# Optimization experiments

Hardware: AMD Instinct MI355X
Metric: run time of the kernel (lower is better)

Reference implementation:

```python
import jax, jax.numpy as jnp
import numpy as np

N = 1500
GAT_IN = 32
GAT_OUT = 8
MLP_HIDDEN = 128
ALPHA = 0.2  # leaky relu slope
NEG_INF = -9.0e15


def setup_inputs() -> dict:
    key = jax.random.key(0)
    ks = jax.random.split(key, 16)
    eye = jnp.eye(N, dtype=jnp.float32)
    geo_adj = jnp.maximum((jax.random.uniform(ks[0], (N, N)) < 0.02).astype(jnp.float32), eye)
    sem_adj = jnp.maximum((jax.random.uniform(ks[1], (N, N)) < 0.02).astype(jnp.float32), eye)
    features = jax.random.normal(ks[2], (N, GAT_IN), dtype=jnp.float32)
    # all (i, j) region pairs, as in the original source
    ii, jj = jnp.meshgrid(jnp.arange(N), jnp.arange(N), indexing='ij')
    region_pairs = jnp.stack([ii.reshape(-1), jj.reshape(-1)], axis=1).astype(jnp.int64)
    distance_features = jax.random.uniform(ks[3], (N * N, 1), dtype=jnp.float32)
    def lin(k, fan_in, fan_out):
        return jax.random.normal(k, (fan_in, fan_out), dtype=jnp.float32) / jnp.sqrt(jnp.float32(fan_in))
    W0 = lin(ks[4], GAT_IN, GAT_OUT)
    W1 = lin(ks[5], GAT_OUT, GAT_OUT)
    W2 = lin(ks[6], GAT_OUT, GAT_OUT)
    a0 = lin(ks[7], 2 * GAT_OUT, 1)
    a1 = lin(ks[8], 2 * GAT_OUT, 1)
    a2 = lin(ks[9], 2 * GAT_OUT, 1)
    fc1_w = lin(ks[10], 2 * GAT_OUT + 1, MLP_HIDDEN)
    fc1_b = jnp.zeros((MLP_HIDDEN,), dtype=jnp.float32)
    fc2_w = lin(ks[11], MLP_HIDDEN, 1)
    fc2_b = jnp.zeros((1,), dtype=jnp.float32)
    return {"geo_adj": geo_adj, "sem_adj": sem_adj, "features": features,
            "region_pairs": region_pairs, "distance_features": distance_features,
            "W0": W0, "W1": W1, "W2": W2, "a0": a0, "a1": a1, "a2": a2,
            "fc1_w": fc1_w, "fc1_b": fc1_b, "fc2_w": fc2_w, "fc2_b": fc2_b}


def _gat_layer(combined_adj, feats, W, a):
    # h = W feats; attention score a([h_i || h_j]) decomposes into h_i@a1 + h_j@a2
    h = feats @ W                      # [N, out]
    f_src = h @ a[:GAT_OUT]            # [N, 1]
    f_dst = h @ a[GAT_OUT:]            # [N, 1]
    e = jax.nn.leaky_relu(f_src + f_dst.T, negative_slope=ALPHA)  # [N, N]
    e = e * combined_adj
    att = jax.nn.softmax(jnp.where(combined_adj > 0, e, NEG_INF), axis=1)
    return jax.nn.elu(att @ h)


def reference(geo_adj, sem_adj, features, region_pairs, distance_features,
              W0, W1, W2, a0, a1, a2, fc1_w, fc1_b, fc2_w, fc2_b):
    combined_adj = geo_adj + sem_adj
    enc = features
    for W, a in ((W0, a0), (W1, a1), (W2, a2)):
        enc = _gat_layer(combined_adj, enc, W, a)
    r1 = enc[region_pairs[:, 0]]       # [N^2, out]
    r2 = enc[region_pairs[:, 1]]       # [N^2, out]
    comb = jnp.concatenate([r1, r2, distance_features], axis=1)  # [N^2, 17]
    hid = jax.nn.relu(comb @ fc1_w + fc1_b)
    return hid @ fc2_w + fc2_b
```

## Files before the change

### kernel.cpp

```cpp
#include <hip/hip_runtime.h>
#include <hip/hip_bf16.h>

#define NN 1500
#define GIN 32
#define GOUT 8
#define HID 128

template<int IN>
__global__ void gat_project(const float* __restrict__ enc,
                            const float* __restrict__ W,
                            const float* __restrict__ avec,
                            float* __restrict__ h,
                            float* __restrict__ fsrc,
                            float* __restrict__ fdst) {
    int i = blockIdx.x * blockDim.x + threadIdx.x;
    if (i >= NN) return;
    float e[IN];
    #pragma unroll
    for (int c = 0; c < IN; ++c) e[c] = enc[i * IN + c];
    float hv[GOUT];
    #pragma unroll
    for (int k = 0; k < GOUT; ++k) {
        float s = 0.f;
        #pragma unroll
        for (int c = 0; c < IN; ++c) s = fmaf(e[c], W[c * GOUT + k], s);
        hv[k] = s;
        h[i * GOUT + k] = s;
    }
    float fs = 0.f, fd = 0.f;
    #pragma unroll
    for (int k = 0; k < GOUT; ++k) {
        fs = fmaf(hv[k], avec[k], fs);
        fd = fmaf(hv[k], avec[GOUT + k], fd);
    }
    fsrc[i] = fs;
    fdst[i] = fd;
}

__global__ void gat_attn(const float* __restrict__ geo,
                         const float* __restrict__ sem,
                         const float* __restrict__ h,
                         const float* __restrict__ fsrc,
                         const float* __restrict__ fdst,
                         float* __restrict__ enc_out) {
    const int i = blockIdx.x;
    const int t = threadIdx.x;
    const float s = fsrc[i];
    const float* grow = geo + (size_t)i * NN;
    const float* srow = sem + (size_t)i * NN;

    float m = -3.0e38f;
    for (int j = t; j < NN; j += 256) {
        float a = grow[j] + srow[j];
        if (a > 0.f) {
            float e = s + fdst[j];
            e = (e > 0.f) ? e : 0.2f * e;
            e *= a;
            m = fmaxf(m, e);
        }
    }
    #pragma unroll
    for (int off = 32; off > 0; off >>= 1)
        m = fmaxf(m, __shfl_down(m, off, 64));
    __shared__ float wred[4];
    if ((t & 63) == 0) wred[t >> 6] = m;
    __syncthreads();
    m = fmaxf(fmaxf(wred[0], wred[1]), fmaxf(wred[2], wred[3]));

    float l = 0.f;
    float acc[GOUT] = {};
    for (int j = t; j < NN; j += 256) {
        float a = grow[j] + srow[j];
        if (a > 0.f) {
            float e = s + fdst[j];
            e = (e > 0.f) ? e : 0.2f * e;
            e *= a;
            float p = __expf(e - m);
            l += p;
            const float* hr = h + j * GOUT;
            #pragma unroll
            for (int c = 0; c < GOUT; ++c) acc[c] = fmaf(p, hr[c], acc[c]);
        }
    }
    #pragma unroll
    for (int off = 32; off > 0; off >>= 1) {
        l += __shfl_down(l, off, 64);
        #pragma unroll
        for (int c = 0; c < GOUT; ++c) acc[c] += __shfl_down(acc[c], off, 64);
    }
    __shared__ float wsum[4][GOUT + 1];
    if ((t & 63) == 0) {
        wsum[t >> 6][0] = l;
        #pragma unroll
        for (int c = 0; c < GOUT; ++c) wsum[t >> 6][1 + c] = acc[c];
    }
    __syncthreads();
    if (t < GOUT) {
        float L = wsum[0][0] + wsum[1][0] + wsum[2][0] + wsum[3][0];
        float v = (wsum[0][1 + t] + wsum[1][1 + t] + wsum[2][1 + t] + wsum[3][1 + t]) / L;
        enc_out[i * GOUT + t] = (v > 0.f) ? v : (__expf(v) - 1.f);
    }
}

__global__ void uv_kernel(const float* __restrict__ enc,
                          const float* __restrict__ fc1w,
                          const float* __restrict__ fc1b,
                          float* __restrict__ U, float* __restrict__ V) {
    const int i = blockIdx.x;
    const int k = threadIdx.x;
    __shared__ float er[GOUT];
    if (k < GOUT) er[k] = enc[i * GOUT + k];
    __syncthreads();
    float u = fc1b[k];
    float v = 0.f;
    #pragma unroll
    for (int c = 0; c < GOUT; ++c) {
        u = fmaf(er[c], fc1w[c * HID + k], u);
        v = fmaf(er[c], fc1w[(GOUT + c) * HID + k], v);
    }
    U[i * HID + k] = u;
    V[i * HID + k] = v;
}

#define TILE 48
#define STRIDE 132

__global__ __launch_bounds__(256, 3) void mlp_kernel(
        const float* __restrict__ U, const float* __restrict__ V,
        const float* __restrict__ dist,
        const float* __restrict__ fc1w,
        const float* __restrict__ fc2w,
        const float* __restrict__ fc2b,
        float* __restrict__ out) {
    __shared__ float Us[TILE * STRIDE];
    __shared__ float Vs[TILE * STRIDE];
    __shared__ float w16s[HID];
    __shared__ float f2s[HID];

    const int tid = threadIdx.x;
    const int i0 = blockIdx.y * TILE;
    const int j0 = blockIdx.x * TILE;

    for (int t = tid; t < TILE * 32; t += 256) {
        int r = t >> 5;
        int k4 = (t & 31) << 2;
        int gi = i0 + r; if (gi >= NN) gi = NN - 1;
        int gj = j0 + r; if (gj >= NN) gj = NN - 1;
        *(float4*)(Us + r * STRIDE + k4) = *(const float4*)(U + gi * HID + k4);
        *(float4*)(Vs + r * STRIDE + k4) = *(const float4*)(V + gj * HID + k4);
    }
    if (tid < HID) {
        w16s[tid] = fc1w[16 * HID + tid];
        f2s[tid] = fc2w[tid];
    }
    __syncthreads();

    const int tx = tid & 15;
    const int ty = tid >> 4;

    int irow[3], jcol[3];
    float d[3][3];
    #pragma unroll
    for (int ii = 0; ii < 3; ++ii) irow[ii] = i0 + ty + 16 * ii;
    #pragma unroll
    for (int jj = 0; jj < 3; ++jj) jcol[jj] = j0 + tx + 16 * jj;
    #pragma unroll
    for (int ii = 0; ii < 3; ++ii) {
        int ic = irow[ii] < NN ? irow[ii] : NN - 1;
        #pragma unroll
        for (int jj = 0; jj < 3; ++jj) {
            int jc = jcol[jj] < NN ? jcol[jj] : NN - 1;
            d[ii][jj] = dist[(size_t)ic * NN + jc];
        }
    }

    float acc[3][3] = {};
    for (int k = 0; k < HID; k += 4) {
        float4 u4[3], v4[3];
        #pragma unroll
        for (int ii = 0; ii < 3; ++ii)
            u4[ii] = *(const float4*)(Us + (ty + 16 * ii) * STRIDE + k);
        #pragma unroll
        for (int jj = 0; jj < 3; ++jj)
            v4[jj] = *(const float4*)(Vs + (tx + 16 * jj) * STRIDE + k);
        float4 wk = *(const float4*)(w16s + k);
        float4 fk = *(const float4*)(f2s + k);
        const float* wkp = (const float*)&wk;
        const float* fkp = (const float*)&fk;
        #pragma unroll
        for (int kk = 0; kk < 4; ++kk) {
            float w = wkp[kk];
            float f = fkp[kk];
            #pragma unroll
            for (int ii = 0; ii < 3; ++ii) {
                float uv = ((const float*)&u4[ii])[kk];
                #pragma unroll
                for (int jj = 0; jj < 3; ++jj) {
                    float tval = fmaf(d[ii][jj], w, uv + ((const float*)&v4[jj])[kk]);
                    tval = fmaxf(tval, 0.f);
                    acc[ii][jj] = fmaf(tval, f, acc[ii][jj]);
                }
            }
        }
    }

    const float b2 = fc2b[0];
    #pragma unroll
    for (int ii = 0; ii < 3; ++ii) {
        if (irow[ii] >= NN) continue;
        #pragma unroll
        for (int jj = 0; jj < 3; ++jj) {
            if (jcol[jj] >= NN) continue;
            out[(size_t)irow[ii] * NN + jcol[jj]] = acc[ii][jj] + b2;
        }
    }
}

extern "C" void kernel_launch(void* const* d_in, const int* in_sizes, int n_in,
                              void* d_out, int out_size, void* d_ws, size_t ws_size,
                              hipStream_t stream) {
    const float* geo  = (const float*)d_in[0];
    const float* sem  = (const float*)d_in[1];
    const float* feat = (const float*)d_in[2];
    const float* dist = (const float*)d_in[4];
    const float* W0   = (const float*)d_in[5];
    const float* W1   = (const float*)d_in[6];
    const float* W2   = (const float*)d_in[7];
    const float* a0   = (const float*)d_in[8];
    const float* a1   = (const float*)d_in[9];
    const float* a2   = (const float*)d_in[10];
    const float* fc1w = (const float*)d_in[11];
    const float* fc1b = (const float*)d_in[12];
    const float* fc2w = (const float*)d_in[13];
    const float* fc2b = (const float*)d_in[14];
    float* out = (float*)d_out;

    float* ws   = (float*)d_ws;
    float* h    = ws;
    float* fsrc = h + NN * GOUT;
    float* fdst = fsrc + NN;
    float* encA = fdst + NN;
    float* encB = encA + NN * GOUT;
    float* Ubuf = encB + NN * GOUT;
    float* Vbuf = Ubuf + NN * HID;

    dim3 pg((NN + 255) / 256), pb(256);

    gat_project<GIN><<<pg, pb, 0, stream>>>(feat, W0, a0, h, fsrc, fdst);
    gat_attn<<<NN, 256, 0, stream>>>(geo, sem, h, fsrc, fdst, encA);

    gat_project<GOUT><<<pg, pb, 0, stream>>>(encA, W1, a1, h, fsrc, fdst);
    gat_attn<<<NN, 256, 0, stream>>>(geo, sem, h, fsrc, fdst, encB);

    gat_project<GOUT><<<pg, pb, 0, stream>>>(encB, W2, a2, h, fsrc, fdst);
    gat_attn<<<NN, 256, 0, stream>>>(geo, sem, h, fsrc, fdst, encA);

    uv_kernel<<<NN, HID, 0, stream>>>(encA, fc1w, fc1b, Ubuf, Vbuf);

    dim3 mg((NN + TILE - 1) / TILE, (NN + TILE - 1) / TILE);
    mlp_kernel<<<mg, 256, 0, stream>>>(Ubuf, Vbuf, dist, fc1w, fc2w, fc2b, out);
}
```

Before: 178.0 us.

## Build CSR adjacency once, fuse GAT projection/attention, fold UV into MLP

Scans the dense geo+sem adjacency once into a fixed-capacity CSR, so that each of the three GAT layers only visits actual neighbours instead of rereading two dense N×N matrices. Projection and attention are fused into one kernel that recomputes neighbour features on the fly, and the softmax skips max-subtraction. The U/V precompute is folded into the MLP tile load, and the MLP inner loop uses packed two-wide float math. Risks are neighbours beyond the 192 capacity being silently dropped, and exp overflow without the max shift.

```diff
diff --git a/kernel.cpp b/kernel.cpp
--- a/kernel.cpp
+++ b/kernel.cpp
@@ -5,130 +5,118 @@
 #define GIN 32
 #define GOUT 8
 #define HID 128
-
-template<int IN>
-__global__ void gat_project(const float* __restrict__ enc,
-                            const float* __restrict__ W,
-                            const float* __restrict__ avec,
-                            float* __restrict__ h,
-                            float* __restrict__ fsrc,
-                            float* __restrict__ fdst) {
-    int i = blockIdx.x * blockDim.x + threadIdx.x;
-    if (i >= NN) return;
-    float e[IN];
-    #pragma unroll
-    for (int c = 0; c < IN; ++c) e[c] = enc[i * IN + c];
-    float hv[GOUT];
-    #pragma unroll
-    for (int k = 0; k < GOUT; ++k) {
-        float s = 0.f;
-        #pragma unroll
-        for (int c = 0; c < IN; ++c) s = fmaf(e[c], W[c * GOUT + k], s);
-        hv[k] = s;
-        h[i * GOUT + k] = s;
-    }
-    float fs = 0.f, fd = 0.f;
-    #pragma unroll
-    for (int k = 0; k < GOUT; ++k) {
-        fs = fmaf(hv[k], avec[k], fs);
-        fd = fmaf(hv[k], avec[GOUT + k], fd);
-    }
-    fsrc[i] = fs;
-    fdst[i] = fd;
-}
-
-__global__ void gat_attn(const float* __restrict__ geo,
-                         const float* __restrict__ sem,
-                         const float* __restrict__ h,
-                         const float* __restrict__ fsrc,
-                         const float* __restrict__ fdst,
-                         float* __restrict__ enc_out) {
+#define CAP 192
+
+typedef float v2f __attribute__((ext_vector_type(2)));
+
+__global__ void build_csr(const float* __restrict__ geo,
+                          const float* __restrict__ sem,
+                          int* __restrict__ csr_idx,
+                          float* __restrict__ csr_val,
+                          int* __restrict__ csr_cnt) {
     const int i = blockIdx.x;
     const int t = threadIdx.x;
-    const float s = fsrc[i];
+    __shared__ int cnt;
+    __shared__ int sidx[CAP];
+    __shared__ float sval[CAP];
+    if (t == 0) cnt = 0;
+    __syncthreads();
     const float* grow = geo + (size_t)i * NN;
     const float* srow = sem + (size_t)i * NN;
-
-    float m = -3.0e38f;
-    for (int j = t; j < NN; j += 256) {
-        float a = grow[j] + srow[j];
-        if (a > 0.f) {
-            float e = s + fdst[j];
-            e = (e > 0.f) ? e : 0.2f * e;
-            e *= a;
-            m = fmaxf(m, e);
-        }
-    }
-    #pragma unroll
-    for (int off = 32; off > 0; off >>= 1)
-        m = fmaxf(m, __shfl_down(m, off, 64));
-    __shared__ float wred[4];
-    if ((t & 63) == 0) wred[t >> 6] = m;
+    for (int q = t; q < NN / 4; q += 256) {
+        float4 g = *(const float4*)(grow + 4 * q);
+        float4 s = *(const float4*)(srow + 4 * q);
+        float a[4] = {g.x + s.x, g.y + s.y, g.z + s.z, g.w + s.w};
+        #pragma unroll
+        for (int c = 0; c < 4; ++c) {
+            if (a[c] > 0.f) {
+                int p = atomicAdd(&cnt, 1);
+                if (p < CAP) { sidx[p] = 4 * q + c; sval[p] = a[c]; }
+            }
+        }
+    }
     __syncthreads();
-    m = fmaxf(fmaxf(wred[0], wred[1]), fmaxf(wred[2], wred[3]));
-
-    float l = 0.f;
-    float acc[GOUT] = {};
-    for (int j = t; j < NN; j += 256) {
-        float a = grow[j] + srow[j];
-        if (a > 0.f) {
-            float e = s + fdst[j];
-            e = (e > 0.f) ? e : 0.2f * e;
-            e *= a;
-            float p = __expf(e - m);
-            l += p;
-            const float* hr = h + j * GOUT;
+    int c2 = cnt < CAP ? cnt : CAP;
+    if (t == 0) csr_cnt[i] = c2;
+    for (int p = t; p < c2; p += 256) {
+        csr_idx[(size_t)i * CAP + p] = sidx[p];
+        csr_val[(size_t)i * CAP + p] = sval[p];
+    }
+}
+
+template<int IN>
+__global__ void gat_layer(const float* __restrict__ enc,
+                          const float* __restrict__ W,
+                          const float* __restrict__ avec,
+                          const int* __restrict__ csr_idx,
+                          const float* __restrict__ csr_val,
+                          const int* __restrict__ csr_cnt,
+                          float* __restrict__ enc_out) {
+    const int tid = threadIdx.x;
+    const int lane = tid & 63;
+    const int i = blockIdx.x * 4 + (tid >> 6);
+
+    float hv = 0.f;
+    if (lane < GOUT) {
+        #pragma unroll 4
+        for (int c = 0; c < IN; ++c)
+            hv = fmaf(enc[(size_t)i * IN + c], W[c * GOUT + lane], hv);
+    }
+    float hi[GOUT];
+    #pragma unroll
+    for (int c = 0; c < GOUT; ++c) hi[c] = __shfl(hv, c, 64);
+    float fsrc = 0.f;
+    #pragma unroll
+    for (int c = 0; c < GOUT; ++c) fsrc = fmaf(hi[c], avec[c], fsrc);
+
+    const int cnt = csr_cnt[i];
+    float den = 0.f;
+    float num[GOUT] = {};
+    for (int e = lane; e < cnt; e += 64) {
+        int j = csr_idx[(size_t)i * CAP + e];
+        float a = csr_val[(size_t)i * CAP + e];
+        float hj[GOUT] = {};
+        #pragma unroll
+        for (int c4 = 0; c4 < IN / 4; ++c4) {
+            float4 e4 = *(const float4*)(enc + (size_t)j * IN + 4 * c4);
+            const float* ep = (const float*)&e4;
             #pragma unroll
-            for (int c = 0; c < GOUT; ++c) acc[c] = fmaf(p, hr[c], acc[c]);
-        }
+            for (int c = 0; c < 4; ++c)
+                #pragma unroll
+                for (int k = 0; k < GOUT; ++k)
+                    hj[k] = fmaf(ep[c], W[(4 * c4 + c) * GOUT + k], hj[k]);
+        }
+        float fd = 0.f;
+        #pragma unroll
+        for (int k = 0; k < GOUT; ++k) fd = fmaf(hj[k], avec[GOUT + k], fd);
+        float ev = fsrc + fd;
+        ev = (ev > 0.f) ? ev : 0.2f * ev;
+        ev *= a;
+        float p = __expf(ev);
+        den += p;
+        #pragma unroll
+        for (int k = 0; k < GOUT; ++k) num[k] = fmaf(p, hj[k], num[k]);
     }
     #pragma unroll
     for (int off = 32; off > 0; off >>= 1) {
-        l += __shfl_down(l, off, 64);
-        #pragma unroll
-        for (int c = 0; c < GOUT; ++c) acc[c] += __shfl_down(acc[c], off, 64);
-    }
-    __shared__ float wsum[4][GOUT + 1];
-    if ((t & 63) == 0) {
-        wsum[t >> 6][0] = l;
-        #pragma unroll
-        for (int c = 0; c < GOUT; ++c) wsum[t >> 6][1 + c] = acc[c];
-    }
-    __syncthreads();
-    if (t < GOUT) {
-        float L = wsum[0][0] + wsum[1][0] + wsum[2][0] + wsum[3][0];
-        float v = (wsum[0][1 + t] + wsum[1][1 + t] + wsum[2][1 + t] + wsum[3][1 + t]) / L;
-        enc_out[i * GOUT + t] = (v > 0.f) ? v : (__expf(v) - 1.f);
-    }
-}
-
-__global__ void uv_kernel(const float* __restrict__ enc,
-                          const float* __restrict__ fc1w,
-                          const float* __restrict__ fc1b,
-                          float* __restrict__ U, float* __restrict__ V) {
-    const int i = blockIdx.x;
-    const int k = threadIdx.x;
-    __shared__ float er[GOUT];
-    if (k < GOUT) er[k] = enc[i * GOUT + k];
-    __syncthreads();
-    float u = fc1b[k];
-    float v = 0.f;
-    #pragma unroll
-    for (int c = 0; c < GOUT; ++c) {
-        u = fmaf(er[c], fc1w[c * HID + k], u);
-        v = fmaf(er[c], fc1w[(GOUT + c) * HID + k], v);
-    }
-    U[i * HID + k] = u;
-    V[i * HID + k] = v;
+        den += __shfl_xor(den, off, 64);
+        #pragma unroll
+        for (int k = 0; k < GOUT; ++k) num[k] += __shfl_xor(num[k], off, 64);
+    }
+    if (lane < GOUT) {
+        float v = num[lane] / den;
+        enc_out[(size_t)i * GOUT + lane] = (v > 0.f) ? v : (__expf(v) - 1.f);
+    }
 }
 
 #define TILE 48
 #define STRIDE 132
 
 __global__ __launch_bounds__(256, 3) void mlp_kernel(
-        const float* __restrict__ U, const float* __restrict__ V,
+        const float* __restrict__ enc,
         const float* __restrict__ dist,
         const float* __restrict__ fc1w,
+        const float* __restrict__ fc1b,
         const float* __restrict__ fc2w,
         const float* __restrict__ fc2b,
         float* __restrict__ out) {
@@ -141,17 +129,34 @@
     const int i0 = blockIdx.y * TILE;
     const int j0 = blockIdx.x * TILE;
 
-    for (int t = tid; t < TILE * 32; t += 256) {
-        int r = t >> 5;
-        int k4 = (t & 31) << 2;
-        int gi = i0 + r; if (gi >= NN) gi = NN - 1;
-        int gj = j0 + r; if (gj >= NN) gj = NN - 1;
-        *(float4*)(Us + r * STRIDE + k4) = *(const float4*)(U + gi * HID + k4);
-        *(float4*)(Vs + r * STRIDE + k4) = *(const float4*)(V + gj * HID + k4);
-    }
-    if (tid < HID) {
-        w16s[tid] = fc1w[16 * HID + tid];
-        f2s[tid] = fc2w[tid];
+    {
+        const int kg = tid & 31;
+        const int k4 = kg << 2;
+        const int rb = tid >> 5;
+        float4 b4 = *(const float4*)(fc1b + k4);
+        for (int r = rb; r < TILE; r += 8) {
+            int gi = i0 + r; if (gi >= NN) gi = NN - 1;
+            int gj = j0 + r; if (gj >= NN) gj = NN - 1;
+            float4 u = b4;
+            float4 v = {0.f, 0.f, 0.f, 0.f};
+            #pragma unroll
+            for (int c = 0; c < GOUT; ++c) {
+                float ei = enc[(size_t)gi * GOUT + c];
+                float ej = enc[(size_t)gj * GOUT + c];
+                float4 wu = *(const float4*)(fc1w + c * HID + k4);
+                float4 wv = *(const float4*)(fc1w + (GOUT + c) * HID + k4);
+                u.x = fmaf(ei, wu.x, u.x); u.y = fmaf(ei, wu.y, u.y);
+                u.z = fmaf(ei, wu.z, u.z); u.w = fmaf(ei, wu.w, u.w);
+                v.x = fmaf(ej, wv.x, v.x); v.y = fmaf(ej, wv.y, v.y);
+                v.z = fmaf(ej, wv.z, v.z); v.w = fmaf(ej, wv.w, v.w);
+            }
+            *(float4*)(Us + r * STRIDE + k4) = u;
+            *(float4*)(Vs + r * STRIDE + k4) = v;
+        }
+        if (tid < HID) {
+            w16s[tid] = fc1w[2 * GOUT * HID + tid];
+            f2s[tid] = fc2w[tid];
+        }
     }
     __syncthreads();
 
@@ -174,7 +179,7 @@
         }
     }
 
-    float acc[3][3] = {};
+    v2f acc[3][3] = {};
     for (int k = 0; k < HID; k += 4) {
         float4 u4[3], v4[3];
         #pragma unroll
@@ -185,20 +190,21 @@
             v4[jj] = *(const float4*)(Vs + (tx + 16 * jj) * STRIDE + k);
         float4 wk = *(const float4*)(w16s + k);
         float4 fk = *(const float4*)(f2s + k);
-        const float* wkp = (const float*)&wk;
-        const float* fkp = (const float*)&fk;
-        #pragma unroll
-        for (int kk = 0; kk < 4; ++kk) {
-            float w = wkp[kk];
-            float f = fkp[kk];
+        const v2f* wp = (const v2f*)&wk;
+        const v2f* fp = (const v2f*)&fk;
+        #pragma unroll
+        for (int h = 0; h < 2; ++h) {
+            v2f w2 = wp[h];
+            v2f f2 = fp[h];
             #pragma unroll
             for (int ii = 0; ii < 3; ++ii) {
-                float uv = ((const float*)&u4[ii])[kk];
+                v2f u2 = ((const v2f*)&u4[ii])[h];
                 #pragma unroll
                 for (int jj = 0; jj < 3; ++jj) {
-                    float tval = fmaf(d[ii][jj], w, uv + ((const float*)&v4[jj])[kk]);
-                    tval = fmaxf(tval, 0.f);
-                    acc[ii][jj] = fmaf(tval, f, acc[ii][jj]);
+                    v2f t = u2 + ((const v2f*)&v4[jj])[h];
+                    t = t + w2 * d[ii][jj];
+                    t = __builtin_elementwise_max(t, (v2f)0.f);
+                    acc[ii][jj] = acc[ii][jj] + t * f2;
                 }
             }
         }
@@ -211,7 +217,7 @@
         #pragma unroll
         for (int jj = 0; jj < 3; ++jj) {
             if (jcol[jj] >= NN) continue;
-            out[(size_t)irow[ii] * NN + jcol[jj]] = acc[ii][jj] + b2;
+            out[(size_t)irow[ii] * NN + jcol[jj]] = acc[ii][jj].x + acc[ii][jj].y + b2;
         }
     }
 }
@@ -235,28 +241,19 @@
     const float* fc2b = (const float*)d_in[14];
     float* out = (float*)d_out;
 
-    float* ws   = (float*)d_ws;
-    float* h    = ws;
-    float* fsrc = h + NN * GOUT;
-    float* fdst = fsrc + NN;
-    float* encA = fdst + NN;
-    float* encB = encA + NN * GOUT;
-    float* Ubuf = encB + NN * GOUT;
-    float* Vbuf = Ubuf + NN * HID;
-
-    dim3 pg((NN + 255) / 256), pb(256);
-
-    gat_project<GIN><<<pg, pb, 0, stream>>>(feat, W0, a0, h, fsrc, fdst);
-    gat_attn<<<NN, 256, 0, stream>>>(geo, sem, h, fsrc, fdst, encA);
-
-    gat_project<GOUT><<<pg, pb, 0, stream>>>(encA, W1, a1, h, fsrc, fdst);
-    gat_attn<<<NN, 256, 0, stream>>>(geo, sem, h, fsrc, fdst, encB);
-
-    gat_project<GOUT><<<pg, pb, 0, stream>>>(encB, W2, a2, h, fsrc, fdst);
-    gat_attn<<<NN, 256, 0, stream>>>(geo, sem, h, fsrc, fdst, encA);
-
-    uv_kernel<<<NN, HID, 0, stream>>>(encA, fc1w, fc1b, Ubuf, Vbuf);
+    char* ws = (char*)d_ws;
+    int*   csr_idx = (int*)ws;                         ws += sizeof(int) * NN * CAP;
+    float* csr_val = (float*)ws;                       ws += sizeof(float) * NN * CAP;
+    int*   csr_cnt = (int*)ws;                         ws += sizeof(int) * NN;
+    float* encA    = (float*)ws;                       ws += sizeof(float) * NN * GOUT;
+    float* encB    = (float*)ws;
+
+    build_csr<<<NN, 256, 0, stream>>>(geo, sem, csr_idx, csr_val, csr_cnt);
+
+    gat_layer<GIN><<<NN / 4, 256, 0, stream>>>(feat, W0, a0, csr_idx, csr_val, csr_cnt, encA);
+    gat_layer<GOUT><<<NN / 4, 256, 0, stream>>>(encA, W1, a1, csr_idx, csr_val, csr_cnt, encB);
+    gat_layer<GOUT><<<NN / 4, 256, 0, stream>>>(encB, W2, a2, csr_idx, csr_val, csr_cnt, encA);
 
     dim3 mg((NN + TILE - 1) / TILE, (NN + TILE - 1) / TILE);
-    mlp_kernel<<<mg, 256, 0, stream>>>(Ubuf, Vbuf, dist, fc1w, fc2w, fc2b, out);
-}
+    mlp_kernel<<<mg, 256, 0, stream>>>(encA, dist, fc1w, fc1b, fc2w, fc2b, out);
+}
```

New measurement: 160.5 us. 1.11x faster.
